# Optimization experiments

Hardware: AMD Instinct MI355X
Metric: run time of the kernel (lower is better)

Reference implementation:

```python
import jax, jax.numpy as jnp
import numpy as np

S, N, F, H, O = 64, 4096, 32, 64, 2  # seq_len, n_nodes, nfeat, nhid, nout


def setup_inputs() -> dict:
    key = jax.random.key(0)
    ks = jax.random.split(key, 8)
    sc = 0.02
    return {
        "x": jax.random.normal(ks[0], (S, N, F), jnp.float32),
        "adj": jax.random.uniform(ks[1], (N, N), jnp.float32) / N,  # dense normalized-ish adjacency
        "W1": jax.random.normal(ks[2], (F, H), jnp.float32) * sc,
        "b1": jnp.zeros((H,), jnp.float32),
        "W2": jax.random.normal(ks[3], (H, O), jnp.float32) * sc,
        "b2": jnp.zeros((O,), jnp.float32),
        "Wih0": jax.random.normal(ks[4], (3 * H, O * N), jnp.float32) * sc,
        "Whh0": jax.random.normal(ks[5], (3 * H, H), jnp.float32) * sc,
        "bih0": jnp.zeros((3 * H,), jnp.float32),
        "bhh0": jnp.zeros((3 * H,), jnp.float32),
        "Wih1": jax.random.normal(ks[6], (3 * H, H), jnp.float32) * sc,
        "Whh1": jax.random.normal(ks[7], (3 * H, H), jnp.float32) * sc,
        "bih1": jnp.zeros((3 * H,), jnp.float32),
        "bhh1": jnp.zeros((3 * H,), jnp.float32),
    }


def _gru_layer(xs, Wih, Whh, bih, bhh):
    # xs: (S, B, in); PyTorch GRU cell semantics, h0 = 0
    B = xs.shape[1]
    h0 = jnp.zeros((B, Whh.shape[1]), xs.dtype)

    def step(h, x_t):
        gi = x_t @ Wih.T + bih            # (B, 3H)
        gh = h @ Whh.T + bhh              # (B, 3H)
        ir, iz, inn = jnp.split(gi, 3, axis=-1)
        hr, hz, hn = jnp.split(gh, 3, axis=-1)
        r = jax.nn.sigmoid(ir + hr)
        z = jax.nn.sigmoid(iz + hz)
        n = jnp.tanh(inn + r * hn)
        h_new = (1.0 - z) * n + z * h
        return h_new, h_new

    hT, ys = jax.lax.scan(step, h0, xs)
    return ys, hT


def reference(x, adj, W1, b1, W2, b2, Wih0, Whh0, bih0, bhh0, Wih1, Whh1, bih1, bhh1):
    # GCN per timestep (vectorized over time): adj @ (x @ W) + b, relu, adj @ (. @ W2) + b2, log_softmax
    # dropout inactive (eval mode)
    support = jnp.einsum('snf,fh->snh', x, W1) + b1          # (S, N, H)
    h = jnp.einsum('ij,sjh->sih', adj, support)              # (S, N, H)
    h = jax.nn.relu(h)
    support2 = jnp.einsum('snh,ho->sno', h, W2) + b2         # (S, N, O)
    g = jnp.einsum('ij,sjo->sio', adj, support2)             # (S, N, O)
    logp = jax.nn.log_softmax(g, axis=-1)                    # dim=1 of (N, O) per node
    rnn_in = logp.reshape(S, 1, N * O)                       # batch = 1 (torch.stack construction)
    ys0, h0T = _gru_layer(rnn_in, Wih0, Whh0, bih0, bhh0)
    ys1, h1T = _gru_layer(ys0, Wih1, Whh1, bih1, bhh1)
    hn = jnp.stack([h0T, h1T])                               # (n_layers, 1, H)
    return ys1, hn
```

## Files before the change

### kernel.cpp

```cpp
#include <hip/hip_runtime.h>
#include <stdint.h>

#define SS 64
#define NN 4096
#define FF 32
#define HH 64
#define OO 2
#define G3 192

typedef float f32x4 __attribute__((ext_vector_type(4)));
typedef short bf16x8 __attribute__((ext_vector_type(8)));
typedef unsigned short u16x8 __attribute__((ext_vector_type(8)));

#define AS1 __attribute__((address_space(1)))
#define AS3 __attribute__((address_space(3)))

__device__ __forceinline__ unsigned short f2bf(float f) {
  union { float f; uint32_t u; } v; v.f = f;
  uint32_t u = v.u;
  uint32_t r = (u + 0x7FFFu + ((u >> 16) & 1u)) >> 16;
  return (unsigned short)r;
}
__device__ __forceinline__ float bf2f(unsigned short s) {
  union { uint32_t u; float f; } v; v.u = ((uint32_t)s) << 16;
  return v.f;
}

__global__ __launch_bounds__(256) void k_prep(const float* __restrict__ adj,
                                              unsigned short* __restrict__ adjb,
                                              float* __restrict__ rowsum,
                                              const float* __restrict__ x,
                                              unsigned short* __restrict__ Xt) {
  __shared__ float xl[64][33];
  __shared__ float ps[4];
  int tid = threadIdx.x;
  if (blockIdx.x < 4096) {
    int row = blockIdx.x;
    const float4* src = (const float4*)(adj + (size_t)row * 4096);
    ushort4* dst = (ushort4*)(adjb + (size_t)row * 4096);
    float sum = 0.f;
    #pragma unroll
    for (int q = 0; q < 4; ++q) {
      int idx = q * 256 + tid;
      float4 v = src[idx];
      ushort4 r;
      r.x = f2bf(v.x); r.y = f2bf(v.y); r.z = f2bf(v.z); r.w = f2bf(v.w);
      dst[idx] = r;
      sum += (v.x + v.y) + (v.z + v.w);
    }
    #pragma unroll
    for (int off = 1; off < 64; off <<= 1) sum += __shfl_xor(sum, off);
    if ((tid & 63) == 0) ps[tid >> 6] = sum;
    __syncthreads();
    if (tid == 0) rowsum[row] = (ps[0] + ps[1]) + (ps[2] + ps[3]);
    return;
  }
  int bs = blockIdx.x - 4096;
  int s = bs >> 6, jb = (bs & 63) << 6;
  const float4* xg = (const float4*)(x + ((size_t)s * NN + jb) * FF);
  #pragma unroll
  for (int ii = 0; ii < 2; ++ii) {
    int idx = tid + ii * 256;
    float4 v = xg[idx];
    int j = idx >> 3, f = (idx & 7) << 2;
    xl[j][f] = v.x; xl[j][f + 1] = v.y; xl[j][f + 2] = v.z; xl[j][f + 3] = v.w;
  }
  __syncthreads();
  int f = tid >> 3, jc = tid & 7;
  u16x8 ov;
  #pragma unroll
  for (int jj = 0; jj < 8; ++jj) ov[jj] = (short)f2bf(xl[jc * 8 + jj][f]);
  *(u16x8*)(Xt + (size_t)(s * 32 + f) * 4096 + jb + jc * 8) = ov;
}

#define SBAR()   asm volatile("s_barrier" ::: "memory")
#define VMCNT6() asm volatile("s_waitcnt vmcnt(6)" ::: "memory")
#define VMCNT0() asm volatile("s_waitcnt vmcnt(0)" ::: "memory")

__global__ __launch_bounds__(512, 2) void k_gemmAX(
    const unsigned short* __restrict__ A,
    const unsigned short* __restrict__ B,
    const float* __restrict__ rowsum,
    const float* __restrict__ W1f,
    const float* __restrict__ b1f,
    const float* __restrict__ W2f,
    const float* __restrict__ b2f,
    unsigned short* __restrict__ B2t) {
  __shared__ __align__(16) char lds[147456];
  __shared__ __align__(16) unsigned short w1t[64 * 40];
  __shared__ float w2l[128];
  __shared__ float b1l[64];
  __shared__ float b2l[2];
  const int tid = threadIdx.x;
  const int wid = tid >> 6, l = tid & 63;
  const int wr2 = wid >> 2, wc2 = wid & 3;

  {
    float4 v = ((const float4*)W1f)[tid];
    int f = tid >> 4, h = (tid & 15) * 4;
    w1t[(h + 0) * 40 + f] = f2bf(v.x);
    w1t[(h + 1) * 40 + f] = f2bf(v.y);
    w1t[(h + 2) * 40 + f] = f2bf(v.z);
    w1t[(h + 3) * 40 + f] = f2bf(v.w);
  }
  if (tid < 32) *(float4*)&w2l[tid * 4] = ((const float4*)W2f)[tid];
  if (tid < 16) *(float4*)&b1l[tid * 4] = ((const float4*)b1f)[tid];
  if (tid < 2) b2l[tid] = b2f[tid];
  __syncthreads();

  int bid = blockIdx.x;
  int swz = (bid & 7) * 32 + (bid >> 3);
  const int i0 = (swz >> 3) * 128;
  const int c0 = (swz & 7) * 256;

  const int aOffC = wr2 * 8192 + (l & 15) * 128;
  const int bOffC = 16384 + wc2 * 8192 + (l & 15) * 128;
  const int colKK0 = (((l >> 4) * 16)) ^ ((l & 7) << 4);
  const int colKK1 = ((64 + (l >> 4) * 16)) ^ ((l & 7) << 4);

  const int srow = tid >> 3;
  const int scol = (((tid & 7) ^ (srow & 7)) << 4);
  const char* gA = (const char*)A + (size_t)(i0 + srow) * 8192 + scol;
  const char* gB = (const char*)B + (size_t)(c0 + srow) * 8192 + scol;
  char* ldsW = (char*)lds + wid * 1024;
  const char* ldsR = (const char*)lds;

  f32x4 acc[4][4];
  #pragma unroll
  for (int m = 0; m < 4; ++m)
    #pragma unroll
    for (int n = 0; n < 4; ++n) acc[m][n] = {0.f, 0.f, 0.f, 0.f};

  bf16x8 af[4][2], bfr[2][2];

#define STAGE6(K2, BOFS) do {                                                        \
    __builtin_amdgcn_global_load_lds((const AS1 void*)(gA + (K2)),                   \
        (AS3 void*)(ldsW + (BOFS)), 16, 0, 0);                                       \
    __builtin_amdgcn_global_load_lds((const AS1 void*)(gA + 524288 + (K2)),          \
        (AS3 void*)(ldsW + (BOFS) + 8192), 16, 0, 0);                                \
    __builtin_amdgcn_global_load_lds((const AS1 void*)(gB + (K2)),                   \
        (AS3 void*)(ldsW + (BOFS) + 16384), 16, 0, 0);                               \
    __builtin_amdgcn_global_load_lds((const AS1 void*)(gB + 524288 + (K2)),          \
        (AS3 void*)(ldsW + (BOFS) + 24576), 16, 0, 0);                               \
    __builtin_amdgcn_global_load_lds((const AS1 void*)(gB + 1048576 + (K2)),         \
        (AS3 void*)(ldsW + (BOFS) + 32768), 16, 0, 0);                               \
    __builtin_amdgcn_global_load_lds((const AS1 void*)(gB + 1572864 + (K2)),         \
        (AS3 void*)(ldsW + (BOFS) + 40960), 16, 0, 0);                               \
  } while (0)

#define READ_AF(BOFS) do {                                                           \
    _Pragma("unroll")                                                                \
    for (int _m = 0; _m < 4; ++_m) {                                                 \
      const char* _p = ldsR + (BOFS) + aOffC + _m * 2048;                            \
      af[_m][0] = *(const bf16x8*)(_p + colKK0);                                     \
      af[_m][1] = *(const bf16x8*)(_p + colKK1);                                     \
    } } while (0)

#define READ_B(BOFS, NH) do {                                                        \
    _Pragma("unroll")                                                                \
    for (int _j = 0; _j < 2; ++_j) {                                                 \
      const char* _p = ldsR + (BOFS) + bOffC + ((NH) * 2 + _j) * 2048;               \
      bfr[_j][0] = *(const bf16x8*)(_p + colKK0);                                    \
      bfr[_j][1] = *(const bf16x8*)(_p + colKK1);                                    \
    } } while (0)

#define MFMA_H(NH) do {                                                              \
    __builtin_amdgcn_s_setprio(1);                                                   \
    _Pragma("unroll")                                                                \
    for (int _kk = 0; _kk < 2; ++_kk)                                                \
      _Pragma("unroll")                                                              \
      for (int _m = 0; _m < 4; ++_m)                                                 \
        _Pragma("unroll")                                                            \
        for (int _j = 0; _j < 2; ++_j)                                               \
          acc[_m][(NH) * 2 + _j] = __builtin_amdgcn_mfma_f32_16x16x32_bf16(          \
              af[_m][_kk], bfr[_j][_kk], acc[_m][(NH) * 2 + _j], 0, 0, 0);           \
    __builtin_amdgcn_s_setprio(0);                                                   \
  } while (0)

  STAGE6(0, 0);
  STAGE6(128, 49152);
  VMCNT6();
  SBAR();

  int bofs = 0, bofs2 = 98304;
  for (int kt = 0; kt < 64; ++kt) {
    const int k2 = ((kt + 2) & 63) * 128;
    READ_AF(bofs);
    READ_B(bofs, 0);
    STAGE6(k2, bofs2);
    MFMA_H(0);
    READ_B(bofs, 1);
    MFMA_H(1);
    VMCNT6();
    SBAR();
    bofs = (bofs == 98304) ? 0 : bofs + 49152;
    bofs2 = (bofs2 == 98304) ? 0 : bofs2 + 49152;
  }
  VMCNT0();
  __syncthreads();

  unsigned short* C1L = (unsigned short*)lds;
  {
    const int rb = wr2 * 64 + (l >> 4) * 4;
    const int cbL = wc2 * 64 + (l & 15);
    #pragma unroll
    for (int m = 0; m < 4; ++m)
      #pragma unroll
      for (int r = 0; r < 4; ++r) {
        const int row = rb + m * 16 + r;
        #pragma unroll
        for (int n = 0; n < 4; ++n)
          C1L[row * 264 + cbL + n * 16] = f2bf(acc[m][n][r]);
      }
  }
  __syncthreads();

  {
    const f32x4 zacc = {0.f, 0.f, 0.f, 0.f};
    const int lc = l & 15, lq = l >> 4;
    bf16x8 bw[4];
    float b1v[4], w2a[4], w2b[4];
    #pragma unroll
    for (int n = 0; n < 4; ++n) {
      const int h = n * 16 + lc;
      bw[n] = *(const bf16x8*)((const char*)w1t + h * 80 + lq * 16);
      b1v[n] = b1l[h];
      w2a[n] = w2l[h * 2];
      w2b[n] = w2l[h * 2 + 1];
    }
    const int rbase = wid * 16 + lq * 4;
    const float4 rs4 = *(const float4*)&rowsum[i0 + rbase];
    const float bo0 = b2l[0], bo1 = b2l[1];
    #pragma unroll
    for (int s = 0; s < 8; ++s) {
      bf16x8 afr = *(const bf16x8*)((const char*)C1L +
                     (wid * 16 + lc) * 528 + s * 64 + lq * 16);
      float o0r[4] = {0.f, 0.f, 0.f, 0.f};
      float o1r[4] = {0.f, 0.f, 0.f, 0.f};
      #pragma unroll
      for (int n = 0; n < 4; ++n) {
        f32x4 hq = __builtin_amdgcn_mfma_f32_16x16x32_bf16(afr, bw[n], zacc, 0, 0, 0);
        #pragma unroll
        for (int r = 0; r < 4; ++r) {
          float hv = hq[r] + rs4[r] * b1v[n];
          hv = hv > 0.f ? hv : 0.f;
          o0r[r] += hv * w2a[n];
          o1r[r] += hv * w2b[n];
        }
      }
      #pragma unroll
      for (int off = 1; off < 16; off <<= 1)
        #pragma unroll
        for (int r = 0; r < 4; ++r) {
          o0r[r] += __shfl_xor(o0r[r], off);
          o1r[r] += __shfl_xor(o1r[r], off);
        }
      if (lc == 0) {
        const int sg = (c0 >> 5) + s;
        #pragma unroll
        for (int r = 0; r < 4; ++r) {
          B2t[(size_t)(sg * 2 + 0) * 4096 + i0 + rbase + r] = f2bf(o0r[r] + bo0);
          B2t[(size_t)(sg * 2 + 1) * 4096 + i0 + rbase + r] = f2bf(o1r[r] + bo1);
        }
      }
    }
  }
}

__device__ __forceinline__ void gemm_core(const unsigned short* __restrict__ A,
                                          const unsigned short* __restrict__ B,
                                          int i0, int c0, int k0base, int ksteps,
                                          f32x4 acc[4][4],
                                          unsigned short* Als, unsigned short* Bls) {
  const int tid = threadIdx.x;
  const int w = tid >> 6, l = tid & 63;
  const int srow = (l >> 2);
  const int scol = (l & 3) * 16;
  for (int kt = 0; kt < ksteps; ++kt) {
    int k0 = k0base + kt * 32;
    #pragma unroll
    for (int q = 0; q < 2; ++q) {
      int r = w * 32 + q * 16 + srow;
      const char* ga = (const char*)(A + (size_t)(i0 + r) * 4096 + k0) + scol;
      __builtin_amdgcn_global_load_lds(
          (const AS1 void*)ga,
          (AS3 void*)((char*)Als + w * 2048 + q * 1024), 16, 0, 0);
      const char* gb = (const char*)(B + (size_t)(c0 + r) * 4096 + k0) + scol;
      __builtin_amdgcn_global_load_lds(
          (const AS1 void*)gb,
          (AS3 void*)((char*)Bls + w * 2048 + q * 1024), 16, 0, 0);
    }
    __syncthreads();
    const int wr = w >> 1, wc = w & 1;
    bf16x8 af[4], bff[4];
    #pragma unroll
    for (int m = 0; m < 4; ++m)
      af[m] = *(const bf16x8*)(Als + (wr * 64 + m * 16 + (l & 15)) * 32 + (l >> 4) * 8);
    #pragma unroll
    for (int n = 0; n < 4; ++n)
      bff[n] = *(const bf16x8*)(Bls + (wc * 64 + n * 16 + (l & 15)) * 32 + (l >> 4) * 8);
    #pragma unroll
    for (int m = 0; m < 4; ++m)
      #pragma unroll
      for (int n = 0; n < 4; ++n)
        acc[m][n] = __builtin_amdgcn_mfma_f32_16x16x32_bf16(af[m], bff[n], acc[m][n], 0, 0, 0);
    __syncthreads();
  }
}

__global__ __launch_bounds__(256) void k_gemm2(const unsigned short* __restrict__ A,
                                               const unsigned short* __restrict__ B,
                                               float* __restrict__ Gp) {
  __shared__ unsigned short Als[128 * 32], Bls[128 * 32];
  int id = blockIdx.x;
  int bi = id & 31, ks = id >> 5;
  int i0 = bi * 128;
  f32x4 acc[4][4];
  #pragma unroll
  for (int m = 0; m < 4; ++m)
    #pragma unroll
    for (int n = 0; n < 4; ++n) acc[m][n] = {0.f, 0.f, 0.f, 0.f};
  gemm_core(A, B, i0, 0, ks * 512, 16, acc, Als, Bls);
  float* outp = Gp + (size_t)ks * 4096 * 128;
  int l = threadIdx.x & 63, w = threadIdx.x >> 6;
  int wr = w >> 1, wc = w & 1;
  int rbase = i0 + wr * 64 + (l >> 4) * 4;
  int cbase = wc * 64 + (l & 15);
  #pragma unroll
  for (int m = 0; m < 4; ++m)
    #pragma unroll
    for (int n = 0; n < 4; ++n)
      #pragma unroll
      for (int r = 0; r < 4; ++r)
        outp[(size_t)(rbase + m * 16 + r) * 128 + cbase + n * 16] = acc[m][n][r];
}

__global__ __launch_bounds__(256) void k_lsm(const float* __restrict__ Gp,
                                             float* __restrict__ Rm) {
  __shared__ float Gacc[32][130];
  int i0 = blockIdx.x * 32;
  int tid = threadIdx.x;
  float4 v[4];
  #pragma unroll
  for (int i = 0; i < 4; ++i) v[i] = {0.f, 0.f, 0.f, 0.f};
  for (int ks = 0; ks < 8; ++ks) {
    const float4* gp4 = ((const float4*)Gp) + (size_t)ks * 131072 + (size_t)i0 * 32;
    #pragma unroll
    for (int i = 0; i < 4; ++i) {
      float4 t = gp4[tid + i * 256];
      v[i].x += t.x; v[i].y += t.y; v[i].z += t.z; v[i].w += t.w;
    }
  }
  #pragma unroll
  for (int i = 0; i < 4; ++i) {
    int f4i = tid + i * 256, row = f4i >> 5, c = (f4i & 31) * 4;
    Gacc[row][c] = v[i].x; Gacc[row][c + 1] = v[i].y;
    Gacc[row][c + 2] = v[i].z; Gacc[row][c + 3] = v[i].w;
  }
  __syncthreads();
  #pragma unroll
  for (int j = 0; j < 8; ++j) {
    int p = j * 256 + tid;
    int ii = p & 31, s = p >> 5;
    float g0 = Gacc[ii][s * 2], g1 = Gacc[ii][s * 2 + 1];
    float m = fmaxf(g0, g1);
    float lse = m + logf(expf(g0 - m) + expf(g1 - m));
    float2 o_; o_.x = g0 - lse; o_.y = g1 - lse;
    *((float2*)(Rm + (size_t)s * 8192 + (size_t)(i0 + ii) * 2)) = o_;
  }
}

__global__ __launch_bounds__(256) void k_gi0(const float* __restrict__ Rm,
                                             const float* __restrict__ Wih0,
                                             float* __restrict__ part) {
  __shared__ float4 Wl[4 * 128];
  int gb = blockIdx.x % 48, ks = blockIdx.x / 48;
  int c0 = ks * 512;
  int tid = threadIdx.x;
  #pragma unroll
  for (int i = 0; i < 2; ++i) {
    int idx = tid + i * 256;
    int g = idx >> 7, c4 = idx & 127;
    Wl[g * 128 + c4] = ((const float4*)(Wih0 + (size_t)(gb * 4 + g) * 8192 + c0))[c4];
  }
  __syncthreads();
  int w = tid >> 6, lane = tid & 63;
  for (int pass = 0; pass < 16; ++pass) {
    int t = pass * 4 + w;
    float a0 = 0.f, a1 = 0.f, a2 = 0.f, a3 = 0.f;
    const float4* rg = (const float4*)(Rm + (size_t)t * 8192 + c0);
    #pragma unroll
    for (int i = 0; i < 2; ++i) {
      int c4 = i * 64 + lane;
      float4 r4 = rg[c4];
      float4 w0 = Wl[c4], w1 = Wl[128 + c4], w2 = Wl[256 + c4], w3 = Wl[384 + c4];
      a0 += r4.x * w0.x + r4.y * w0.y + r4.z * w0.z + r4.w * w0.w;
      a1 += r4.x * w1.x + r4.y * w1.y + r4.z * w1.z + r4.w * w1.w;
      a2 += r4.x * w2.x + r4.y * w2.y + r4.z * w2.z + r4.w * w2.w;
      a3 += r4.x * w3.x + r4.y * w3.y + r4.z * w3.z + r4.w * w3.w;
    }
    #pragma unroll
    for (int off = 1; off < 64; off <<= 1) {
      a0 += __shfl_xor(a0, off);
      a1 += __shfl_xor(a1, off);
      a2 += __shfl_xor(a2, off);
      a3 += __shfl_xor(a3, off);
    }
    if (lane == 0) {
      float4 o_; o_.x = a0; o_.y = a1; o_.z = a2; o_.w = a3;
      *((float4*)(part + ((size_t)ks * 64 + t) * 192 + gb * 4)) = o_;
    }
  }
}

__global__ __launch_bounds__(256) void k_gi0red(const float* __restrict__ part,
                                                const float* __restrict__ bih0,
                                                float* __restrict__ gi0) {
  int idx = blockIdx.x * 256 + threadIdx.x;
  if (idx < 12288) {
    float s_ = bih0[idx % 192];
    for (int ks = 0; ks < 16; ++ks) s_ += part[ks * 12288 + idx];
    gi0[idx] = s_;
  }
}

__device__ __forceinline__ float fsigm(float x) {
  return __builtin_amdgcn_rcpf(1.f + __expf(-x));
}
__device__ __forceinline__ float ftanh(float x) {
  return 1.f - 2.f * __builtin_amdgcn_rcpf(1.f + __expf(2.f * x));
}

__global__ __launch_bounds__(384) void k_gru(const float* __restrict__ gi0,
                                             const float* __restrict__ Whh0,
                                             const float* __restrict__ bhh0,
                                             const float* __restrict__ Wih1,
                                             const float* __restrict__ Whh1,
                                             const float* __restrict__ bih1,
                                             const float* __restrict__ bhh1,
                                             float* __restrict__ out) {
  __shared__ float gil[64][192];
  __shared__ float gout[576];
  __shared__ __align__(16) unsigned short hv[2][64];
  const int tid = threadIdx.x;
  const int w = tid >> 6, l = tid & 63;
  const int matw = w >> 1, half = w & 1;
  const float* Wm = (matw == 0) ? Whh0 : (matw == 1 ? Wih1 : Whh1);
  const int mi = (matw == 2) ? 1 : 0;

  bf16x8 afr[6][2];
  #pragma unroll
  for (int rbi = 0; rbi < 6; ++rbi) {
    int g = (half * 6 + rbi) * 16 + (l & 15);
    #pragma unroll
    for (int kh = 0; kh < 2; ++kh) {
      int k0 = kh * 32 + (l >> 4) * 8;
      const float4* src = (const float4*)(Wm + (size_t)g * 64 + k0);
      float4 v0 = src[0], v1 = src[1];
      bf16x8 a;
      a[0] = (short)f2bf(v0.x); a[1] = (short)f2bf(v0.y);
      a[2] = (short)f2bf(v0.z); a[3] = (short)f2bf(v0.w);
      a[4] = (short)f2bf(v1.x); a[5] = (short)f2bf(v1.y);
      a[6] = (short)f2bf(v1.z); a[7] = (short)f2bf(v1.w);
      afr[rbi][kh] = a;
    }
  }
  {
    float4* gf = (float4*)&gil[0][0];
    const float4* gs = (const float4*)gi0;
    #pragma unroll
    for (int i = 0; i < 8; ++i) gf[i * 384 + tid] = gs[i * 384 + tid];
  }
  if (tid < 128) hv[tid >> 6][tid & 63] = 0;

  float hreg = 0.f;
  float bR = 0.f, bZ = 0.f, bNa = 0.f, bNb = 0.f;
  if (tid < 64) {
    bR = bhh0[tid]; bZ = bhh0[64 + tid]; bNa = bhh0[128 + tid];
  } else if (tid < 128) {
    int g = tid - 64;
    bR = bih1[g] + bhh1[g];
    bZ = bih1[64 + g] + bhh1[64 + g];
    bNa = bih1[128 + g];
    bNb = bhh1[128 + g];
  }
  asm volatile("s_waitcnt lgkmcnt(0)\n\ts_barrier" ::: "memory");

  const int gwb = matw * 192 + half * 96 + (l >> 4) * 4;
  const f32x4 zacc = {0.f, 0.f, 0.f, 0.f};

  for (int i = 0; i <= 64; ++i) {
    bf16x8 b0 = *(const bf16x8*)&hv[mi][(l >> 4) * 8];
    bf16x8 b1 = *(const bf16x8*)&hv[mi][32 + (l >> 4) * 8];
    #pragma unroll
    for (int rbi = 0; rbi < 6; ++rbi) {
      f32x4 a_ = __builtin_amdgcn_mfma_f32_16x16x32_bf16(afr[rbi][0], b0, zacc, 0, 0, 0);
      a_ = __builtin_amdgcn_mfma_f32_16x16x32_bf16(afr[rbi][1], b1, a_, 0, 0, 0);
      if (!(l & 15)) *(f32x4*)&gout[gwb + rbi * 16] = a_;
    }
    asm volatile("s_waitcnt lgkmcnt(0)\n\ts_barrier" ::: "memory");
    if (tid < 64) {
      if (i < 64) {
        float r = fsigm(gil[i][tid] + gout[tid] + bR);
        float z = fsigm(gil[i][64 + tid] + gout[64 + tid] + bZ);
        float n = ftanh(gil[i][128 + tid] + r * (gout[128 + tid] + bNa));
        hreg = (1.f - z) * n + z * hreg;
        hv[0][tid] = f2bf(hreg);
      }
    } else if (tid < 128 && i > 0) {
      int g = tid - 64;
      float r = fsigm(gout[192 + g] + gout[384 + g] + bR);
      float z = fsigm(gout[256 + g] + gout[448 + g] + bZ);
      float n = ftanh((gout[320 + g] + bNa) + r * (gout[512 + g] + bNb));
      hreg = (1.f - z) * n + z * hreg;
      hv[1][g] = f2bf(hreg);
      out[(i - 1) * 64 + g] = hreg;
    }
    asm volatile("s_waitcnt lgkmcnt(0)\n\ts_barrier" ::: "memory");
  }
  if (tid < 64) out[4096 + tid] = hreg;
  else if (tid < 128) out[4096 + 64 + (tid - 64)] = hreg;
}

extern "C" void kernel_launch(void* const* d_in, const int* in_sizes, int n_in,
                              void* d_out, int out_size, void* d_ws, size_t ws_size,
                              hipStream_t stream) {
  const float* x    = (const float*)d_in[0];
  const float* adj  = (const float*)d_in[1];
  const float* W1   = (const float*)d_in[2];
  const float* b1   = (const float*)d_in[3];
  const float* W2   = (const float*)d_in[4];
  const float* b2   = (const float*)d_in[5];
  const float* Wih0 = (const float*)d_in[6];
  const float* Whh0 = (const float*)d_in[7];
  const float* bih0 = (const float*)d_in[8];
  const float* bhh0 = (const float*)d_in[9];
  const float* Wih1 = (const float*)d_in[10];
  const float* Whh1 = (const float*)d_in[11];
  const float* bih1 = (const float*)d_in[12];
  const float* bhh1 = (const float*)d_in[13];
  float* out = (float*)d_out;

  char* ws = (char*)d_ws;
  unsigned short* adjb = (unsigned short*)ws;
  unsigned short* Xt   = (unsigned short*)(ws + 33554432);
  float* rowsum        = (float*)(ws + 67108864);
  float* Gp            = (float*)(ws + 67125248);
  float* Rm            = (float*)(ws + 83902464);
  float* part          = (float*)(ws + 85999616);
  float* gi0           = (float*)(ws + 86786048);
  unsigned short* B2t  = (unsigned short*)(ws + 86835200);

  k_prep<<<8192, 256, 0, stream>>>(adj, adjb, rowsum, x, Xt);
  k_gemmAX<<<256, 512, 0, stream>>>(adjb, Xt, rowsum, W1, b1, W2, b2, B2t);
  k_gemm2<<<256, 256, 0, stream>>>(adjb, B2t, Gp);
  k_lsm<<<128, 256, 0, stream>>>(Gp, Rm);
  k_gi0<<<768, 256, 0, stream>>>(Rm, Wih0, part);
  k_gi0red<<<48, 256, 0, stream>>>(part, bih0, gi0);
  k_gru<<<1, 384, 0, stream>>>(gi0, Whh0, bhh0, Wih1, Whh1, bih1, bhh1, out);
}
```

Before: 176.0 us.

## Switch adj@X GEMM to FP8 e4m3 MFMA with scaled adjacency and 4-stage pipeline

```diff
diff --git a/kernel.cpp b/kernel.cpp
--- a/kernel.cpp
+++ b/kernel.cpp
@@ -25,12 +25,27 @@
   union { uint32_t u; float f; } v; v.u = ((uint32_t)s) << 16;
   return v.f;
 }
+__device__ __forceinline__ unsigned char f2e4m3(float x) {
+  float a = fabsf(x);
+  unsigned s = (x < 0.f) ? 0x80u : 0u;
+  if (a >= 448.f) return (unsigned char)(s | 0x7E);
+  if (a < 0.015625f) {
+    int q = (int)rintf(a * 512.f);
+    return (unsigned char)(s | (unsigned)q);
+  }
+  union { float f; uint32_t u; } v; v.f = a;
+  uint32_t b = v.u + 0x7FFFFu + ((v.u >> 20) & 1u);
+  int e = (int)(b >> 23) - 127;
+  if (e > 8) return (unsigned char)(s | 0x7E);
+  return (unsigned char)(s | (unsigned)(((e + 7) << 3) | ((b >> 20) & 7u)));
+}
 
 __global__ __launch_bounds__(256) void k_prep(const float* __restrict__ adj,
                                               unsigned short* __restrict__ adjb,
+                                              unsigned char* __restrict__ adj8,
                                               float* __restrict__ rowsum,
                                               const float* __restrict__ x,
-                                              unsigned short* __restrict__ Xt) {
+                                              unsigned char* __restrict__ Xt8) {
   __shared__ float xl[64][33];
   __shared__ float ps[4];
   int tid = threadIdx.x;
@@ -38,6 +53,7 @@
     int row = blockIdx.x;
     const float4* src = (const float4*)(adj + (size_t)row * 4096);
     ushort4* dst = (ushort4*)(adjb + (size_t)row * 4096);
+    uchar4* dst8 = (uchar4*)(adj8 + (size_t)row * 4096);
     float sum = 0.f;
     #pragma unroll
     for (int q = 0; q < 4; ++q) {
@@ -46,6 +62,10 @@
       ushort4 r;
       r.x = f2bf(v.x); r.y = f2bf(v.y); r.z = f2bf(v.z); r.w = f2bf(v.w);
       dst[idx] = r;
+      uchar4 r8;
+      r8.x = f2e4m3(v.x * 4096.f); r8.y = f2e4m3(v.y * 4096.f);
+      r8.z = f2e4m3(v.z * 4096.f); r8.w = f2e4m3(v.w * 4096.f);
+      dst8[idx] = r8;
       sum += (v.x + v.y) + (v.z + v.w);
     }
     #pragma unroll
@@ -67,26 +87,31 @@
   }
   __syncthreads();
   int f = tid >> 3, jc = tid & 7;
-  u16x8 ov;
-  #pragma unroll
-  for (int jj = 0; jj < 8; ++jj) ov[jj] = (short)f2bf(xl[jc * 8 + jj][f]);
-  *(u16x8*)(Xt + (size_t)(s * 32 + f) * 4096 + jb + jc * 8) = ov;
+  unsigned int lo = 0, hi = 0;
+  #pragma unroll
+  for (int jj = 0; jj < 4; ++jj) lo |= ((unsigned int)f2e4m3(xl[jc * 8 + jj][f])) << (jj * 8);
+  #pragma unroll
+  for (int jj = 0; jj < 4; ++jj) hi |= ((unsigned int)f2e4m3(xl[jc * 8 + 4 + jj][f])) << (jj * 8);
+  uint2 ov; ov.x = lo; ov.y = hi;
+  *(uint2*)(Xt8 + (size_t)(s * 32 + f) * 4096 + jb + jc * 8) = ov;
 }
 
 #define SBAR()   asm volatile("s_barrier" ::: "memory")
-#define VMCNT6() asm volatile("s_waitcnt vmcnt(6)" ::: "memory")
-#define VMCNT0() asm volatile("s_waitcnt vmcnt(0)" ::: "memory")
+#define VMC9()   asm volatile("s_waitcnt vmcnt(9)" ::: "memory")
+#define VMC6()   asm volatile("s_waitcnt vmcnt(6)" ::: "memory")
+#define VMC3()   asm volatile("s_waitcnt vmcnt(3)" ::: "memory")
+#define VMC0()   asm volatile("s_waitcnt vmcnt(0)" ::: "memory")
 
 __global__ __launch_bounds__(512, 2) void k_gemmAX(
-    const unsigned short* __restrict__ A,
-    const unsigned short* __restrict__ B,
+    const unsigned char* __restrict__ A8,
+    const unsigned char* __restrict__ B8,
     const float* __restrict__ rowsum,
     const float* __restrict__ W1f,
     const float* __restrict__ b1f,
     const float* __restrict__ W2f,
     const float* __restrict__ b2f,
     unsigned short* __restrict__ B2t) {
-  __shared__ __align__(16) char lds[147456];
+  __shared__ __align__(16) char lds[122880];
   __shared__ __align__(16) unsigned short w1t[64 * 40];
   __shared__ float w2l[128];
   __shared__ float b1l[64];
@@ -94,6 +119,7 @@
   const int tid = threadIdx.x;
   const int wid = tid >> 6, l = tid & 63;
   const int wr2 = wid >> 2, wc2 = wid & 3;
+  const int lc = l & 15, lq = l >> 4;
 
   {
     float4 v = ((const float4*)W1f)[tid];
@@ -113,15 +139,17 @@
   const int i0 = (swz >> 3) * 128;
   const int c0 = (swz & 7) * 256;
 
-  const int aOffC = wr2 * 8192 + (l & 15) * 128;
-  const int bOffC = 16384 + wc2 * 8192 + (l & 15) * 128;
-  const int colKK0 = (((l >> 4) * 16)) ^ ((l & 7) << 4);
-  const int colKK1 = ((64 + (l >> 4) * 16)) ^ ((l & 7) << 4);
-
-  const int srow = tid >> 3;
-  const int scol = (((tid & 7) ^ (srow & 7)) << 4);
-  const char* gA = (const char*)A + (size_t)(i0 + srow) * 8192 + scol;
-  const char* gB = (const char*)B + (size_t)(c0 + srow) * 8192 + scol;
+  const int aBase = (wr2 * 64 + lc) * 64;
+  const int bBase = 8192 + (wc2 * 64 + lc) * 64;
+  const int aswz = (lc & 3) ^ ((lc >> 2) & 3);
+  const int ck0 = ((((lq >> 1)) ^ aswz) << 4) + (lq & 1) * 8;
+  const int ck1 = (((2 + (lq >> 1)) ^ aswz) << 4) + (lq & 1) * 8;
+
+  const int srow = wid * 16 + (l >> 2);
+  const int sswz = (srow & 3) ^ ((srow >> 2) & 3);
+  const int scol = (((l & 3) ^ sswz) << 4);
+  const char* gA = (const char*)A8 + (size_t)(i0 + srow) * 4096 + scol;
+  const char* gB = (const char*)B8 + (size_t)(c0 + srow) * 4096 + scol;
   char* ldsW = (char*)lds + wid * 1024;
   const char* ldsR = (const char*)lds;
 
@@ -131,78 +159,71 @@
     #pragma unroll
     for (int n = 0; n < 4; ++n) acc[m][n] = {0.f, 0.f, 0.f, 0.f};
 
-  bf16x8 af[4][2], bfr[2][2];
-
-#define STAGE6(K2, BOFS) do {                                                        \
-    __builtin_amdgcn_global_load_lds((const AS1 void*)(gA + (K2)),                   \
+  long afr[4][2], bfr[4][2];
+
+#define STAGE3(KT, BOFS) do {                                                        \
+    __builtin_amdgcn_global_load_lds((const AS1 void*)(gA + (KT) * 64),              \
         (AS3 void*)(ldsW + (BOFS)), 16, 0, 0);                                       \
-    __builtin_amdgcn_global_load_lds((const AS1 void*)(gA + 524288 + (K2)),          \
+    __builtin_amdgcn_global_load_lds((const AS1 void*)(gB + (KT) * 64),              \
         (AS3 void*)(ldsW + (BOFS) + 8192), 16, 0, 0);                                \
-    __builtin_amdgcn_global_load_lds((const AS1 void*)(gB + (K2)),                   \
+    __builtin_amdgcn_global_load_lds((const AS1 void*)(gB + 524288 + (KT) * 64),     \
         (AS3 void*)(ldsW + (BOFS) + 16384), 16, 0, 0);                               \
-    __builtin_amdgcn_global_load_lds((const AS1 void*)(gB + 524288 + (K2)),          \
-        (AS3 void*)(ldsW + (BOFS) + 24576), 16, 0, 0);                               \
-    __builtin_amdgcn_global_load_lds((const AS1 void*)(gB + 1048576 + (K2)),         \
-        (AS3 void*)(ldsW + (BOFS) + 32768), 16, 0, 0);                               \
-    __builtin_amdgcn_global_load_lds((const AS1 void*)(gB + 1572864 + (K2)),         \
-        (AS3 void*)(ldsW + (BOFS) + 40960), 16, 0, 0);                               \
   } while (0)
 
-#define READ_AF(BOFS) do {                                                           \
+#define READ_FR(BOFS) do {                                                           \
     _Pragma("unroll")                                                                \
     for (int _m = 0; _m < 4; ++_m) {                                                 \
-      const char* _p = ldsR + (BOFS) + aOffC + _m * 2048;                            \
-      af[_m][0] = *(const bf16x8*)(_p + colKK0);                                     \
-      af[_m][1] = *(const bf16x8*)(_p + colKK1);                                     \
+      const char* _p = ldsR + (BOFS) + aBase + _m * 1024;                            \
+      afr[_m][0] = *(const long*)(_p + ck0);                                         \
+      afr[_m][1] = *(const long*)(_p + ck1);                                         \
+    }                                                                                \
+    _Pragma("unroll")                                                                \
+    for (int _n = 0; _n < 4; ++_n) {                                                 \
+      const char* _q = ldsR + (BOFS) + bBase + _n * 1024;                            \
+      bfr[_n][0] = *(const long*)(_q + ck0);                                         \
+      bfr[_n][1] = *(const long*)(_q + ck1);                                         \
     } } while (0)
 
-#define READ_B(BOFS, NH) do {                                                        \
-    _Pragma("unroll")                                                                \
-    for (int _j = 0; _j < 2; ++_j) {                                                 \
-      const char* _p = ldsR + (BOFS) + bOffC + ((NH) * 2 + _j) * 2048;               \
-      bfr[_j][0] = *(const bf16x8*)(_p + colKK0);                                    \
-      bfr[_j][1] = *(const bf16x8*)(_p + colKK1);                                    \
-    } } while (0)
-
-#define MFMA_H(NH) do {                                                              \
+#define MFMA32() do {                                                                \
     __builtin_amdgcn_s_setprio(1);                                                   \
     _Pragma("unroll")                                                                \
     for (int _kk = 0; _kk < 2; ++_kk)                                                \
       _Pragma("unroll")                                                              \
       for (int _m = 0; _m < 4; ++_m)                                                 \
         _Pragma("unroll")                                                            \
-        for (int _j = 0; _j < 2; ++_j)                                               \
-          acc[_m][(NH) * 2 + _j] = __builtin_amdgcn_mfma_f32_16x16x32_bf16(          \
-              af[_m][_kk], bfr[_j][_kk], acc[_m][(NH) * 2 + _j], 0, 0, 0);           \
+        for (int _n = 0; _n < 4; ++_n)                                               \
+          acc[_m][_n] = __builtin_amdgcn_mfma_f32_16x16x32_fp8_fp8(                  \
+              afr[_m][_kk], bfr[_n][_kk], acc[_m][_n], 0, 0, 0);                     \
     __builtin_amdgcn_s_setprio(0);                                                   \
   } while (0)
 
-  STAGE6(0, 0);
-  STAGE6(128, 49152);
-  VMCNT6();
+  STAGE3(0, 0);
+  STAGE3(1, 24576);
+  STAGE3(2, 49152);
+  STAGE3(3, 73728);
+  VMC9();
   SBAR();
 
-  int bofs = 0, bofs2 = 98304;
-  for (int kt = 0; kt < 64; ++kt) {
-    const int k2 = ((kt + 2) & 63) * 128;
-    READ_AF(bofs);
-    READ_B(bofs, 0);
-    STAGE6(k2, bofs2);
-    MFMA_H(0);
-    READ_B(bofs, 1);
-    MFMA_H(1);
-    VMCNT6();
+  int bR = 0, bS = 98304;
+  for (int kt = 0; kt < 60; ++kt) {
+    READ_FR(bR);
+    STAGE3(kt + 4, bS);
+    MFMA32();
+    VMC9();
     SBAR();
-    bofs = (bofs == 98304) ? 0 : bofs + 49152;
-    bofs2 = (bofs2 == 98304) ? 0 : bofs2 + 49152;
-  }
-  VMCNT0();
+    bR = (bR == 98304) ? 0 : bR + 24576;
+    bS = (bS == 98304) ? 0 : bS + 24576;
+  }
+  READ_FR(bR); MFMA32(); VMC6(); SBAR(); bR = (bR == 98304) ? 0 : bR + 24576;
+  READ_FR(bR); MFMA32(); VMC3(); SBAR(); bR = (bR == 98304) ? 0 : bR + 24576;
+  READ_FR(bR); MFMA32(); VMC0(); SBAR(); bR = (bR == 98304) ? 0 : bR + 24576;
+  READ_FR(bR); MFMA32();
   __syncthreads();
 
   unsigned short* C1L = (unsigned short*)lds;
   {
-    const int rb = wr2 * 64 + (l >> 4) * 4;
-    const int cbL = wc2 * 64 + (l & 15);
+    const int rb = wr2 * 64 + lq * 4;
+    const int cbL = wc2 * 64 + lc;
     #pragma unroll
     for (int m = 0; m < 4; ++m)
       #pragma unroll
@@ -210,14 +231,13 @@
         const int row = rb + m * 16 + r;
         #pragma unroll
         for (int n = 0; n < 4; ++n)
-          C1L[row * 264 + cbL + n * 16] = f2bf(acc[m][n][r]);
+          C1L[row * 264 + cbL + n * 16] = f2bf(acc[m][n][r] * 0.000244140625f);
       }
   }
   __syncthreads();
 
   {
     const f32x4 zacc = {0.f, 0.f, 0.f, 0.f};
-    const int lc = l & 15, lq = l >> 4;
     bf16x8 bw[4];
     float b1v[4], w2a[4], w2b[4];
     #pragma unroll
@@ -233,13 +253,13 @@
     const float bo0 = b2l[0], bo1 = b2l[1];
     #pragma unroll
     for (int s = 0; s < 8; ++s) {
-      bf16x8 afr = *(const bf16x8*)((const char*)C1L +
+      bf16x8 afe = *(const bf16x8*)((const char*)C1L +
                      (wid * 16 + lc) * 528 + s * 64 + lq * 16);
       float o0r[4] = {0.f, 0.f, 0.f, 0.f};
       float o1r[4] = {0.f, 0.f, 0.f, 0.f};
       #pragma unroll
       for (int n = 0; n < 4; ++n) {
-        f32x4 hq = __builtin_amdgcn_mfma_f32_16x16x32_bf16(afr, bw[n], zacc, 0, 0, 0);
+        f32x4 hq = __builtin_amdgcn_mfma_f32_16x16x32_bf16(afe, bw[n], zacc, 0, 0, 0);
         #pragma unroll
         for (int r = 0; r < 4; ++r) {
           float hv = hq[r] + rs4[r] * b1v[n];
@@ -543,16 +563,17 @@
 
   char* ws = (char*)d_ws;
   unsigned short* adjb = (unsigned short*)ws;
-  unsigned short* Xt   = (unsigned short*)(ws + 33554432);
-  float* rowsum        = (float*)(ws + 67108864);
-  float* Gp            = (float*)(ws + 67125248);
-  float* Rm            = (float*)(ws + 83902464);
-  float* part          = (float*)(ws + 85999616);
-  float* gi0           = (float*)(ws + 86786048);
-  unsigned short* B2t  = (unsigned short*)(ws + 86835200);
-
-  k_prep<<<8192, 256, 0, stream>>>(adj, adjb, rowsum, x, Xt);
-  k_gemmAX<<<256, 512, 0, stream>>>(adjb, Xt, rowsum, W1, b1, W2, b2, B2t);
+  unsigned char* adj8  = (unsigned char*)(ws + 33554432);
+  unsigned char* Xt8   = (unsigned char*)(ws + 50331648);
+  float* rowsum        = (float*)(ws + 58720256);
+  float* Gp            = (float*)(ws + 58736640);
+  float* Rm            = (float*)(ws + 75513856);
+  float* part          = (float*)(ws + 77611008);
+  float* gi0           = (float*)(ws + 78397440);
+  unsigned short* B2t  = (unsigned short*)(ws + 78446592);
+
+  k_prep<<<8192, 256, 0, stream>>>(adj, adjb, adj8, rowsum, x, Xt8);
+  k_gemmAX<<<256, 512, 0, stream>>>(adj8, Xt8, rowsum, W1, b1, W2, b2, B2t);
   k_gemm2<<<256, 256, 0, stream>>>(adjb, B2t, Gp);
   k_lsm<<<128, 256, 0, stream>>>(Gp, Rm);
   k_gi0<<<768, 256, 0, stream>>>(Rm, Wih0, part);
```

Measured after the change: 165.5 us. -6.0%, faster.
